# Optimization experiments

Hardware: AMD Instinct MI355X
Metric: run time of the kernel (lower is better)

## Reference

```python
import jax, jax.numpy as jnp
import numpy as np

K = 7            # involution kernel size
GC = 16          # group_channels (fixed in module)
BN_EPS = 1e-5


def setup_inputs() -> dict:
    key = jax.random.key(0)
    ks = jax.random.split(key, 9)
    B, C, H, W = 4, 256, 64, 64
    OUT = 256
    CR = C // 4                     # reduction_ratio = 4
    G = C // GC                     # groups = 16
    x = jax.random.normal(ks[0], (B, C, H, W), dtype=jnp.float32)
    # conv1: 1x1 conv C -> C//4, no bias (followed by BN)
    w1 = jax.random.normal(ks[1], (CR, C), dtype=jnp.float32) * (1.0 / np.sqrt(C))
    gamma = jax.random.uniform(ks[2], (CR,), dtype=jnp.float32, minval=0.5, maxval=1.5)
    beta = jax.random.normal(ks[3], (CR,), dtype=jnp.float32) * 0.1
    mean = jax.random.normal(ks[4], (CR,), dtype=jnp.float32) * 0.1
    var = jax.random.uniform(ks[5], (CR,), dtype=jnp.float32, minval=0.5, maxval=1.5)
    # conv2: 1x1 conv C//4 -> K^2 * groups, with bias
    w2 = jax.random.normal(ks[6], (K * K * G, CR), dtype=jnp.float32) * (1.0 / np.sqrt(CR))
    b2 = jax.random.normal(ks[7], (K * K * G,), dtype=jnp.float32) * 0.01
    # pointwise: 1x1 conv C -> OUT, no bias
    wp = jax.random.normal(ks[8], (OUT, C), dtype=jnp.float32) * (1.0 / np.sqrt(C))
    return {"x": x, "w1": w1, "gamma": gamma, "beta": beta, "mean": mean,
            "var": var, "w2": w2, "b2": b2, "wp": wp}


def reference(x, w1, gamma, beta, mean, var, w2, b2, wp):
    b, c, h, w = x.shape
    groups = c // GC
    # weight-generation branch: 1x1 conv -> BN (inference) -> ReLU -> 1x1 conv
    y = jnp.einsum('oc,bchw->bohw', w1, x)
    scale = (gamma * jax.lax.rsqrt(var + BN_EPS))[None, :, None, None]
    y = jax.nn.relu((y - mean[None, :, None, None]) * scale + beta[None, :, None, None])
    wt = jnp.einsum('oc,bchw->bohw', w2, y) + b2[None, :, None, None]
    wt = wt.reshape(b, groups, 1, K * K, h, w)
    # unfold: (b, c*K*K, h, w) with channel-major ordering (matches torch Unfold)
    p = (K - 1) // 2
    patches = jax.lax.conv_general_dilated_patches(
        x, (K, K), (1, 1), ((p, p), (p, p)))
    patches = patches.reshape(b, groups, GC, K * K, h, w)
    out = (wt * patches).sum(axis=3).reshape(b, c, h, w)
    return jnp.einsum('oc,bchw->bohw', wp, out)
```

## Files before the change

kernel.cpp:

```cpp
#include <hip/hip_runtime.h>

typedef __attribute__((ext_vector_type(8))) short bf16x8;
typedef __attribute__((ext_vector_type(4))) float f32x4;
typedef __attribute__((ext_vector_type(8))) _Float16 h16x8;
typedef unsigned short u16;
typedef unsigned int u32;

__device__ __forceinline__ u16 f2bf(float f) {
    u32 x = __builtin_bit_cast(u32, f);
    return (u16)((x + 0x7fffu + ((x >> 16) & 1u)) >> 16);
}
__device__ __forceinline__ u16 f2h(float f) {
    _Float16 h = (_Float16)f;
    return __builtin_bit_cast(u16, h);
}

__global__ __launch_bounds__(512) void gemm1m_k(
    const float* __restrict__ x,
    const float* __restrict__ w1, const float* __restrict__ gamma,
    const float* __restrict__ beta, const float* __restrict__ mean,
    const float* __restrict__ var,
    u16* __restrict__ ypk)
{
    __shared__ u16 Ws[32 * 64 * 8];
    __shared__ u16 As[2][8 * 64 * 8];

    const int t = threadIdx.x, lane = t & 63, wave = t >> 6;
    const int b = blockIdx.y, n0 = blockIdx.x * 64;
    const int ln = lane & 15, lk = lane >> 4;
    const int wm = wave >> 1, wn = wave & 1;
    const float* xb = x + (size_t)b * 256 * 4096;

    for (int s = t; s < 2048; s += 512) {
        int kg = s >> 6, m = s & 63;
        float sc = gamma[m] * rsqrtf(var[m] + 1e-5f);
        const float4 f0 = *reinterpret_cast<const float4*>(&w1[(size_t)m * 256 + kg * 8]);
        const float4 f1 = *reinterpret_cast<const float4*>(&w1[(size_t)m * 256 + kg * 8 + 4]);
        uint4 v;
        v.x = (u32)f2bf(f0.x * sc) | ((u32)f2bf(f0.y * sc) << 16);
        v.y = (u32)f2bf(f0.z * sc) | ((u32)f2bf(f0.w * sc) << 16);
        v.z = (u32)f2bf(f1.x * sc) | ((u32)f2bf(f1.y * sc) << 16);
        v.w = (u32)f2bf(f1.z * sc) | ((u32)f2bf(f1.w * sc) << 16);
        *reinterpret_cast<uint4*>(&Ws[((kg * 64) + (m ^ (kg & 7))) * 8]) = v;
    }

    const int skg = t >> 6, snn = t & 63;
    float rx[8];
#pragma unroll
    for (int j = 0; j < 8; ++j)
        rx[j] = xb[(size_t)(skg * 8 + j) * 4096 + n0 + snn];
    {
        uint4 v;
        v.x = (u32)f2bf(rx[0]) | ((u32)f2bf(rx[1]) << 16);
        v.y = (u32)f2bf(rx[2]) | ((u32)f2bf(rx[3]) << 16);
        v.z = (u32)f2bf(rx[4]) | ((u32)f2bf(rx[5]) << 16);
        v.w = (u32)f2bf(rx[6]) | ((u32)f2bf(rx[7]) << 16);
        *reinterpret_cast<uint4*>(&As[0][((skg * 64) + (snn ^ skg)) * 8]) = v;
    }
    __syncthreads();

    f32x4 acc[2];
#pragma unroll
    for (int i = 0; i < 2; ++i)
#pragma unroll
        for (int e = 0; e < 4; ++e) acc[i][e] = 0.f;

    for (int ks = 0; ks < 4; ++ks) {
        const int cur = ks & 1;
        if (ks < 3) {
#pragma unroll
            for (int j = 0; j < 8; ++j)
                rx[j] = xb[(size_t)((ks + 1) * 64 + skg * 8 + j) * 4096 + n0 + snn];
        }
#pragma unroll
        for (int k32 = 0; k32 < 2; ++k32) {
            const int kgl = k32 * 4 + lk;
            const int kgw = ks * 8 + kgl;
            const bf16x8 aw = *reinterpret_cast<const bf16x8*>(
                &Ws[((kgw * 64) + ((wm * 16 + ln) ^ (kgw & 7))) * 8]);
#pragma unroll
            for (int i = 0; i < 2; ++i) {
                const int n = wn * 32 + i * 16 + ln;
                const bf16x8 bx = *reinterpret_cast<const bf16x8*>(
                    &As[cur][((kgl * 64) + (n ^ kgl)) * 8]);
                acc[i] = __builtin_amdgcn_mfma_f32_16x16x32_bf16(aw, bx, acc[i], 0, 0, 0);
            }
        }
        if (ks < 3) {
            uint4 v;
            v.x = (u32)f2bf(rx[0]) | ((u32)f2bf(rx[1]) << 16);
            v.y = (u32)f2bf(rx[2]) | ((u32)f2bf(rx[3]) << 16);
            v.z = (u32)f2bf(rx[4]) | ((u32)f2bf(rx[5]) << 16);
            v.w = (u32)f2bf(rx[6]) | ((u32)f2bf(rx[7]) << 16);
            *reinterpret_cast<uint4*>(&As[cur ^ 1][((skg * 64) + (snn ^ skg)) * 8]) = v;
            __syncthreads();
        }
    }

    const int mb = wm * 16 + lk * 4;
    const float4 g4 = *reinterpret_cast<const float4*>(&gamma[mb]);
    const float4 v4 = *reinterpret_cast<const float4*>(&var[mb]);
    const float4 be4 = *reinterpret_cast<const float4*>(&beta[mb]);
    const float4 mn4 = *reinterpret_cast<const float4*>(&mean[mb]);
    float bv[4];
    bv[0] = be4.x - mn4.x * (g4.x * rsqrtf(v4.x + 1e-5f));
    bv[1] = be4.y - mn4.y * (g4.y * rsqrtf(v4.y + 1e-5f));
    bv[2] = be4.z - mn4.z * (g4.z * rsqrtf(v4.z + 1e-5f));
    bv[3] = be4.w - mn4.w * (g4.w * rsqrtf(v4.w + 1e-5f));
    const int kg = mb >> 3, joff = mb & 7;
#pragma unroll
    for (int i = 0; i < 2; ++i) {
        const int n = n0 + wn * 32 + i * 16 + ln;
        u16 p[4];
#pragma unroll
        for (int r = 0; r < 4; ++r)
            p[r] = f2bf(fmaxf(acc[i][r] + bv[r], 0.f));
        uint2 v;
        v.x = (u32)p[0] | ((u32)p[1] << 16);
        v.y = (u32)p[2] | ((u32)p[3] << 16);
        *reinterpret_cast<uint2*>(
            &ypk[(((size_t)b * 8 + kg) * 4096 + n) * 8 + joff]) = v;
    }
}

__global__ __launch_bounds__(512, 4) void fusedinv_k(
    const u16* __restrict__ ypk, const float* __restrict__ w2,
    const float* __restrict__ b2, const float* __restrict__ x,
    u16* __restrict__ invpk)
{
    __shared__ alignas(16) char Lds[66560];
    u16* As = (u16*)Lds;
    u16* Ws = (u16*)(Lds + 32768);
    _Float16* xs = (_Float16*)Lds;
    u16* wt16 = (u16*)(Lds + 40960);

    const int t = threadIdx.x, lane = t & 63, wave = t >> 6;
    const int tile = blockIdx.x, g = blockIdx.y, b = blockIdx.z;
    const int ty0 = (tile >> 2) * 16, tx0 = (tile & 3) * 16;
    const int ln = lane & 15, lk = lane >> 4;
    const int q = wave >> 1, h = wave & 1;

    const u16* yb = ypk + (size_t)b * 8 * 4096 * 8;
#pragma unroll
    for (int r = 0; r < 4; ++r) {
        int s = r * 512 + t;
        int kg = s >> 8, n = s & 255;
        int gpix = (ty0 + (n >> 4)) * 64 + tx0 + (n & 15);
        *reinterpret_cast<uint4*>(&As[((kg * 256) + (n ^ kg)) * 8]) =
            *reinterpret_cast<const uint4*>(&yb[((size_t)kg * 4096 + gpix) * 8]);
    }
    {
        int kg = t >> 6, m = t & 63;
        uint4 v = {0u, 0u, 0u, 0u};
        if (m < 49) {
            const float4 f0 = *reinterpret_cast<const float4*>(
                &w2[(size_t)(g * 49 + m) * 64 + kg * 8]);
            const float4 f1 = *reinterpret_cast<const float4*>(
                &w2[(size_t)(g * 49 + m) * 64 + kg * 8 + 4]);
            v.x = (u32)f2bf(f0.x) | ((u32)f2bf(f0.y) << 16);
            v.y = (u32)f2bf(f0.z) | ((u32)f2bf(f0.w) << 16);
            v.z = (u32)f2bf(f1.x) | ((u32)f2bf(f1.y) << 16);
            v.w = (u32)f2bf(f1.z) | ((u32)f2bf(f1.w) << 16);
        }
        *reinterpret_cast<uint4*>(&Ws[((kg * 64) + (m ^ kg)) * 8]) = v;
    }
    __syncthreads();

    f32x4 acc[8];
#pragma unroll
    for (int i = 0; i < 8; ++i)
#pragma unroll
        for (int e = 0; e < 4; ++e) acc[i][e] = 0.f;

#pragma unroll
    for (int k32 = 0; k32 < 2; ++k32) {
        const int kg = k32 * 4 + lk;
        const bf16x8 wf = *reinterpret_cast<const bf16x8*>(
            &Ws[((kg * 64) + ((q * 16 + ln) ^ kg)) * 8]);
#pragma unroll
        for (int i = 0; i < 8; ++i) {
            const int n = (h * 8 + i) * 16 + ln;
            const bf16x8 af = *reinterpret_cast<const bf16x8*>(
                &As[((kg * 256) + (n ^ kg)) * 8]);
            acc[i] = __builtin_amdgcn_mfma_f32_16x16x32_bf16(af, wf, acc[i], 0, 0, 0);
        }
    }
    __syncthreads();

    const int kk = q * 16 + ln;
    if (kk < 49) {
        const float bv = b2[g * 49 + kk];
#pragma unroll
        for (int i = 0; i < 8; ++i) {
            u16 h0 = f2h(acc[i][0] + bv), h1 = f2h(acc[i][1] + bv);
            u16 h2 = f2h(acc[i][2] + bv), h3 = f2h(acc[i][3] + bv);
            uint2 v;
            v.x = (u32)h0 | ((u32)h1 << 16);
            v.y = (u32)h2 | ((u32)h3 << 16);
            *reinterpret_cast<uint2*>(&wt16[kk * 260 + (h * 8 + i) * 16 + lk * 4]) = v;
        }
    }

    const float* xb = x + (size_t)(b * 256 + g * 16) * 4096;
    for (int idx = t; idx < 968; idx += 512) {
        int plane = idx / 484, sp = idx - plane * 484;
        int sy = sp / 22, sx = sp - sy * 22;
        int gy = ty0 + sy - 3, gx = tx0 + sx - 3;
        uint4 hh = {0u, 0u, 0u, 0u};
        if ((unsigned)gy < 64u && (unsigned)gx < 64u) {
            const float* xp = &xb[(size_t)(plane * 8) * 4096 + gy * 64 + gx];
            float f[8];
#pragma unroll
            for (int j = 0; j < 8; ++j) f[j] = xp[(size_t)j * 4096];
            hh.x = (u32)f2h(f[0]) | ((u32)f2h(f[1]) << 16);
            hh.y = (u32)f2h(f[2]) | ((u32)f2h(f[3]) << 16);
            hh.z = (u32)f2h(f[4]) | ((u32)f2h(f[5]) << 16);
            hh.w = (u32)f2h(f[6]) | ((u32)f2h(f[7]) << 16);
        }
        *reinterpret_cast<uint4*>(&xs[((size_t)plane * 484 + sp) * 8]) = hh;
    }
    __syncthreads();

    const int px = t & 255, half = t >> 8;
    const int py = px >> 4, pxx = px & 15;
    float o[8];
#pragma unroll
    for (int i = 0; i < 8; ++i) o[i] = 0.f;

    for (int dy = 0; dy < 7; ++dy) {
        const int rowb = (py + dy) * 22 + pxx;
#pragma unroll
        for (int dx = 0; dx < 7; ++dx) {
            const int kkx = dy * 7 + dx;
            const float wf = (float)__builtin_bit_cast(_Float16, wt16[kkx * 260 + px]);
            const h16x8 xv = *reinterpret_cast<const h16x8*>(
                &xs[((size_t)half * 484 + rowb + dx) * 8]);
#pragma unroll
            for (int c = 0; c < 8; ++c)
                o[c] += wf * (float)xv[c];
        }
    }

    const int pix = (ty0 + py) * 64 + tx0 + pxx;
    u16 p[8];
#pragma unroll
    for (int j = 0; j < 8; ++j) p[j] = f2bf(o[j]);
    uint4 v;
    v.x = (u32)p[0] | ((u32)p[1] << 16);
    v.y = (u32)p[2] | ((u32)p[3] << 16);
    v.z = (u32)p[4] | ((u32)p[5] << 16);
    v.w = (u32)p[6] | ((u32)p[7] << 16);
    *reinterpret_cast<uint4*>(
        &invpk[(((size_t)b * 32 + g * 2 + half) * 4096 + pix) * 8]) = v;
}

__global__ __launch_bounds__(512, 4) void mgemm4_k(
    const u16* __restrict__ Apk,
    const float* __restrict__ wp,
    float* __restrict__ Cout)
{
    __shared__ u16 As[2][8 * 128 * 8];
    __shared__ u16 Ws[32 * 64 * 8];

    const int t = threadIdx.x;
    const int lane = t & 63, wave = t >> 6;
    const int m0 = blockIdx.x * 64;
    const int batch = blockIdx.y >> 5;
    const int n0 = (blockIdx.y & 31) * 128;
    const u16* Ab = Apk + (size_t)batch * 32 * 4096 * 8;

    const int wn = wave & 3, wm = wave >> 2;
    const int ln = lane & 15, lk = lane >> 4;

    for (int s = t; s < 2048; s += 512) {
        int kg = s >> 6, m = s & 63;
        const float4 f0 = *reinterpret_cast<const float4*>(
            &wp[(size_t)(m0 + m) * 256 + kg * 8]);
        const float4 f1 = *reinterpret_cast<const float4*>(
            &wp[(size_t)(m0 + m) * 256 + kg * 8 + 4]);
        uint4 v;
        v.x = (u32)f2bf(f0.x) | ((u32)f2bf(f0.y) << 16);
        v.y = (u32)f2bf(f0.z) | ((u32)f2bf(f0.w) << 16);
        v.z = (u32)f2bf(f1.x) | ((u32)f2bf(f1.y) << 16);
        v.w = (u32)f2bf(f1.z) | ((u32)f2bf(f1.w) << 16);
        *reinterpret_cast<uint4*>(&Ws[((size_t)kg * 64 + (m ^ (kg & 7))) * 8]) = v;
    }

    uint4 rs[2];
#pragma unroll
    for (int r = 0; r < 2; ++r) {
        int s = r * 512 + t, kg = s >> 7, nn = s & 127;
        rs[r] = *reinterpret_cast<const uint4*>(&Ab[((size_t)kg * 4096 + n0 + nn) * 8]);
    }
#pragma unroll
    for (int r = 0; r < 2; ++r) {
        int s = r * 512 + t, kg = s >> 7, nn = s & 127;
        *reinterpret_cast<uint4*>(&As[0][((size_t)kg * 128 + (nn ^ kg)) * 8]) = rs[r];
    }
    __syncthreads();

    f32x4 acc[2][2];
#pragma unroll
    for (int i = 0; i < 2; ++i)
#pragma unroll
        for (int f = 0; f < 2; ++f)
#pragma unroll
            for (int e = 0; e < 4; ++e) acc[i][f][e] = 0.f;

    for (int ks = 0; ks < 4; ++ks) {
        const int cur = ks & 1;
        if (ks < 3) {
#pragma unroll
            for (int r = 0; r < 2; ++r) {
                int s = r * 512 + t, kg = s >> 7, nn = s & 127;
                rs[r] = *reinterpret_cast<const uint4*>(
                    &Ab[(((size_t)(ks + 1) * 8 + kg) * 4096 + n0 + nn) * 8]);
            }
        }
#pragma unroll
        for (int k32 = 0; k32 < 2; ++k32) {
            const int kg = k32 * 4 + lk;
            const int kgw = ks * 8 + kg;
            bf16x8 a[2], bfr[2];
#pragma unroll
            for (int i = 0; i < 2; ++i) {
                int n = wn * 32 + i * 16 + ln;
                a[i] = *reinterpret_cast<const bf16x8*>(
                    &As[cur][((size_t)kg * 128 + (n ^ kg)) * 8]);
            }
#pragma unroll
            for (int f = 0; f < 2; ++f) {
                int m = wm * 32 + f * 16 + ln;
                bfr[f] = *reinterpret_cast<const bf16x8*>(
                    &Ws[((size_t)kgw * 64 + (m ^ (kgw & 7))) * 8]);
            }
#pragma unroll
            for (int i = 0; i < 2; ++i)
#pragma unroll
                for (int f = 0; f < 2; ++f)
                    acc[i][f] = __builtin_amdgcn_mfma_f32_16x16x32_bf16(
                        a[i], bfr[f], acc[i][f], 0, 0, 0);
        }
        if (ks < 3) {
#pragma unroll
            for (int r = 0; r < 2; ++r) {
                int s = r * 512 + t, kg = s >> 7, nn = s & 127;
                *reinterpret_cast<uint4*>(
                    &As[cur ^ 1][((size_t)kg * 128 + (nn ^ kg)) * 8]) = rs[r];
            }
            __syncthreads();
        }
    }

#pragma unroll
    for (int f = 0; f < 2; ++f) {
        const int m = m0 + wm * 32 + f * 16 + ln;
#pragma unroll
        for (int i = 0; i < 2; ++i) {
            const int n = n0 + wn * 32 + i * 16 + lk * 4;
            float4 v = {acc[i][f][0], acc[i][f][1], acc[i][f][2], acc[i][f][3]};
            *reinterpret_cast<float4*>(&Cout[((size_t)batch * 256 + m) * 4096 + n]) = v;
        }
    }
}

extern "C" void kernel_launch(void* const* d_in, const int* in_sizes, int n_in,
                              void* d_out, int out_size, void* d_ws, size_t ws_size,
                              hipStream_t stream)
{
    const float* x     = (const float*)d_in[0];
    const float* w1    = (const float*)d_in[1];
    const float* gamma = (const float*)d_in[2];
    const float* beta  = (const float*)d_in[3];
    const float* mean  = (const float*)d_in[4];
    const float* var   = (const float*)d_in[5];
    const float* w2    = (const float*)d_in[6];
    const float* b2    = (const float*)d_in[7];
    const float* wp    = (const float*)d_in[8];
    float* out = (float*)d_out;

    u16* u = (u16*)d_ws;
    u16* ypk   = u;
    u16* invpk = u + 1048576;

    gemm1m_k<<<dim3(64, 4), 512, 0, stream>>>(x, w1, gamma, beta, mean, var, ypk);
    fusedinv_k<<<dim3(16, 16, 4), 512, 0, stream>>>(ypk, w2, b2, x, invpk);
    mgemm4_k<<<dim3(4, 128), 512, 0, stream>>>(invpk, wp, out);
}
```

Measured before the change: 49.03 us.

## Compute two adjacent pixels per thread in involution with swizzled LDS reuse

The involution stage now gives each thread two horizontally adjacent pixels and four channels instead of one pixel and eight channels. Each thread loads a row of eight x vectors from LDS once per dy and reuses them across both pixels. The f16 staging buffer gets an XOR swizzle keyed on row to reduce LDS bank conflicts, and the per-kernel weights for both pixels are read as one 32-bit load. Launch bounds drop from 4 to 2 waves per SIMD, which allows more registers per thread but may lower occupancy.

Result: slower. 52.15 us (+6.4%).

```diff
diff --git a/kernel.cpp b/kernel.cpp
--- a/kernel.cpp
+++ b/kernel.cpp
@@ -2,7 +2,7 @@
 
 typedef __attribute__((ext_vector_type(8))) short bf16x8;
 typedef __attribute__((ext_vector_type(4))) float f32x4;
-typedef __attribute__((ext_vector_type(8))) _Float16 h16x8;
+typedef __attribute__((ext_vector_type(4))) _Float16 h16x4;
 typedef unsigned short u16;
 typedef unsigned int u32;
 
@@ -13,6 +13,9 @@
 __device__ __forceinline__ u16 f2h(float f) {
     _Float16 h = (_Float16)f;
     return __builtin_bit_cast(u16, h);
+}
+__device__ __forceinline__ float h2f(u16 u) {
+    return (float)__builtin_bit_cast(_Float16, u);
 }
 
 __global__ __launch_bounds__(512) void gemm1m_k(
@@ -123,7 +126,7 @@
     }
 }
 
-__global__ __launch_bounds__(512, 4) void fusedinv_k(
+__global__ __launch_bounds__(512, 2) void fusedinv_k(
     const u16* __restrict__ ypk, const float* __restrict__ w2,
     const float* __restrict__ b2, const float* __restrict__ x,
     u16* __restrict__ invpk)
@@ -131,7 +134,6 @@
     __shared__ alignas(16) char Lds[66560];
     u16* As = (u16*)Lds;
     u16* Ws = (u16*)(Lds + 32768);
-    _Float16* xs = (_Float16*)Lds;
     u16* wt16 = (u16*)(Lds + 40960);
 
     const int t = threadIdx.x, lane = t & 63, wave = t >> 6;
@@ -187,9 +189,9 @@
     }
     __syncthreads();
 
-    const int kk = q * 16 + ln;
-    if (kk < 49) {
-        const float bv = b2[g * 49 + kk];
+    const int kk0 = q * 16 + ln;
+    if (kk0 < 49) {
+        const float bv = b2[g * 49 + kk0];
 #pragma unroll
         for (int i = 0; i < 8; ++i) {
             u16 h0 = f2h(acc[i][0] + bv), h1 = f2h(acc[i][1] + bv);
@@ -197,7 +199,7 @@
             uint2 v;
             v.x = (u32)h0 | ((u32)h1 << 16);
             v.y = (u32)h2 | ((u32)h3 << 16);
-            *reinterpret_cast<uint2*>(&wt16[kk * 260 + (h * 8 + i) * 16 + lk * 4]) = v;
+            *reinterpret_cast<uint2*>(&wt16[kk0 * 260 + (h * 8 + i) * 16 + lk * 4]) = v;
         }
     }
 
@@ -217,41 +219,58 @@
             hh.z = (u32)f2h(f[4]) | ((u32)f2h(f[5]) << 16);
             hh.w = (u32)f2h(f[6]) | ((u32)f2h(f[7]) << 16);
         }
-        *reinterpret_cast<uint4*>(&xs[((size_t)plane * 484 + sp) * 8]) = hh;
+        const size_t base = (size_t)(plane * 484 + sp) * 16;
+        const size_t key = (size_t)((sy & 7) << 3);
+        *reinterpret_cast<uint2*>((size_t)(Lds) + ((base) ^ key)) = uint2{hh.x, hh.y};
+        *reinterpret_cast<uint2*>((size_t)(Lds) + ((base + 8) ^ key)) = uint2{hh.z, hh.w};
     }
     __syncthreads();
 
-    const int px = t & 255, half = t >> 8;
-    const int py = px >> 4, pxx = px & 15;
-    float o[8];
-#pragma unroll
-    for (int i = 0; i < 8; ++i) o[i] = 0.f;
+    const int pp = t & 127, qq = t >> 7;
+    const int plane = qq >> 1, cq = qq & 1;
+    const int px0 = pp * 2;
+    const int py = px0 >> 4, pxx = px0 & 15;
+
+    float o0[4] = {0.f, 0.f, 0.f, 0.f};
+    float o1[4] = {0.f, 0.f, 0.f, 0.f};
 
     for (int dy = 0; dy < 7; ++dy) {
-        const int rowb = (py + dy) * 22 + pxx;
+        const int sy = py + dy;
+        const size_t rowbase = ((size_t)(plane * 484 + sy * 22 + pxx) * 16) + cq * 8;
+        const size_t key = (size_t)((sy & 7) << 3);
+        h16x4 xv[8];
+#pragma unroll
+        for (int r = 0; r < 8; ++r) {
+            uint2 u = *reinterpret_cast<const uint2*>(
+                (size_t)(Lds) + ((rowbase + (size_t)r * 16) ^ key));
+            xv[r] = __builtin_bit_cast(h16x4, u);
+        }
 #pragma unroll
         for (int dx = 0; dx < 7; ++dx) {
-            const int kkx = dy * 7 + dx;
-            const float wf = (float)__builtin_bit_cast(_Float16, wt16[kkx * 260 + px]);
-            const h16x8 xv = *reinterpret_cast<const h16x8*>(
-                &xs[((size_t)half * 484 + rowb + dx) * 8]);
-#pragma unroll
-            for (int c = 0; c < 8; ++c)
-                o[c] += wf * (float)xv[c];
+            const int kk = dy * 7 + dx;
+            const u32 wpair = *reinterpret_cast<const u32*>(&wt16[kk * 260 + px0]);
+            const float w0 = h2f((u16)(wpair & 0xffffu));
+            const float w1 = h2f((u16)(wpair >> 16));
+#pragma unroll
+            for (int c = 0; c < 4; ++c) {
+                o0[c] += w0 * (float)xv[dx][c];
+                o1[c] += w1 * (float)xv[dx + 1][c];
+            }
         }
     }
 
     const int pix = (ty0 + py) * 64 + tx0 + pxx;
-    u16 p[8];
-#pragma unroll
-    for (int j = 0; j < 8; ++j) p[j] = f2bf(o[j]);
-    uint4 v;
-    v.x = (u32)p[0] | ((u32)p[1] << 16);
-    v.y = (u32)p[2] | ((u32)p[3] << 16);
-    v.z = (u32)p[4] | ((u32)p[5] << 16);
-    v.w = (u32)p[6] | ((u32)p[7] << 16);
-    *reinterpret_cast<uint4*>(
-        &invpk[(((size_t)b * 32 + g * 2 + half) * 4096 + pix) * 8]) = v;
+    u16* ob = invpk + (((size_t)b * 32 + g * 2 + plane) * 4096 + pix) * 8 + cq * 4;
+    {
+        uint2 v;
+        v.x = (u32)f2bf(o0[0]) | ((u32)f2bf(o0[1]) << 16);
+        v.y = (u32)f2bf(o0[2]) | ((u32)f2bf(o0[3]) << 16);
+        *reinterpret_cast<uint2*>(ob) = v;
+        uint2 w;
+        w.x = (u32)f2bf(o1[0]) | ((u32)f2bf(o1[1]) << 16);
+        w.y = (u32)f2bf(o1[2]) | ((u32)f2bf(o1[3]) << 16);
+        *reinterpret_cast<uint2*>(ob + 8) = w;
+    }
 }
 
 __global__ __launch_bounds__(512, 4) void mgemm4_k(
```
